# Kernel optimization log

Measured on AMD Instinct MI355X. Metric: run time of the kernel, lower is better.

Reference implementation:

```python
import jax, jax.numpy as jnp
import numpy as np

B, N, H, HEADS, PH, VD = 32, 256, 768, 12, 128, 16
DH = H // HEADS
VOCAB = 2 * VD + 3


def layer_norm(x, g, b, eps=1e-5):
    m = jnp.mean(x, axis=-1, keepdims=True)
    v = jnp.mean((x - m) ** 2, axis=-1, keepdims=True)
    return (x - m) * jax.lax.rsqrt(v + eps) * g + b


def setup_inputs() -> dict:
    key = jax.random.key(0)
    ks = jax.random.split(key, 12)
    # clamped relative-distance index pool, as in PathEmbeddingDistance
    t = np.arange(N)
    pool = t[None, :] - t[:, None]
    pool = np.clip(pool, -VD - 1, VD + 1) + VD + 1  # in [0, 2*VD+2]
    s = 0.02
    return {
        "nodes": jax.random.normal(ks[0], (B, N, H), jnp.float32),
        "bias": jnp.zeros((B, 1, 1, N), jnp.float32),
        "path_pool": jnp.asarray(pool, jnp.int32),
        "pos_table": jax.random.normal(ks[1], (VOCAB, PH), jnp.float32) * s,
        "Wq": jax.random.normal(ks[2], (H, H), jnp.float32) * s, "bq": jnp.zeros((H,), jnp.float32),
        "Wk": jax.random.normal(ks[3], (H, H), jnp.float32) * s, "bk": jnp.zeros((H,), jnp.float32),
        "Wv": jax.random.normal(ks[4], (H, H), jnp.float32) * s, "bv": jnp.zeros((H,), jnp.float32),
        "Wsk": jax.random.normal(ks[5], (PH, DH), jnp.float32) * s, "bsk": jnp.zeros((DH,), jnp.float32),
        "Wsv": jax.random.normal(ks[6], (PH, DH), jnp.float32) * s, "bsv": jnp.zeros((DH,), jnp.float32),
        "Wo": jax.random.normal(ks[7], (H, H), jnp.float32) * s, "bo": jnp.zeros((H,), jnp.float32),
        "g_path": jnp.ones((PH,), jnp.float32), "b_path": jnp.zeros((PH,), jnp.float32),
        "g_norm": jnp.ones((H,), jnp.float32), "b_norm": jnp.zeros((H,), jnp.float32),
    }


def reference(nodes, bias, path_pool, pos_table, Wq, bq, Wk, bk, Wv, bv,
              Wsk, bsk, Wsv, bsv, Wo, bo, g_path, b_path, g_norm, b_norm):
    # path embedding lookup (batch-independent: torch expand == broadcast)
    paths = pos_table[path_pool]                      # (N, N, PH)
    paths = layer_norm(paths, g_path, b_path)
    q = (nodes @ Wq + bq).reshape(B, N, HEADS, DH).transpose(0, 2, 1, 3)
    k = (nodes @ Wk + bk).reshape(B, N, HEADS, DH).transpose(0, 2, 1, 3)
    v = (nodes @ Wv + bv).reshape(B, N, HEADS, DH).transpose(0, 2, 1, 3)
    struct_k = paths @ Wsk + bsk                      # (N, N, DH)
    struct_v = paths @ Wsv + bsv                      # (N, N, DH)
    q = q * (DH ** -0.5)
    w = jnp.einsum("bhid,bhjd->bhij", q, k)
    struct_w = jnp.einsum("bhid,ijd->bhij", q, struct_k)
    w = jax.nn.softmax(w + struct_w + bias, axis=-1)  # (B, HEADS, N, N)
    out = jnp.einsum("bhij,bhjd->bhid", w, v) + jnp.einsum("bhij,ijd->bhid", w, struct_v)
    out = out.transpose(0, 2, 1, 3).reshape(B, N, H)  # combine heads
    out = jax.nn.relu(out @ Wo + bo)
    return layer_norm(nodes + out, g_norm, b_norm), w
```

## Files before the change

### kernel.cpp

```cpp
#include <hip/hip_runtime.h>
#include <hip/hip_bf16.h>

#define BB 32
#define NN 256
#define HH 768
#define NHEADS 12
#define DH 64
#define PHDIM 128
#define NVOCAB 35

typedef short bf16x8 __attribute__((ext_vector_type(8)));
typedef float f32x16 __attribute__((ext_vector_type(16)));
typedef unsigned u32x2 __attribute__((ext_vector_type(2)));

#define MFMA32 __builtin_amdgcn_mfma_f32_32x32x16_bf16

__device__ __forceinline__ unsigned short f2bf(float f) {
    unsigned u = __float_as_uint(f);
    unsigned r = (u + 0x7fffu + ((u >> 16) & 1u)) >> 16;
    return (unsigned short)r;
}

__device__ __forceinline__ unsigned pk2(float a, float b) {
    return (unsigned)f2bf(a) | ((unsigned)f2bf(b) << 16);
}

__device__ __forceinline__ bf16x8 pack8(const float f[8]) {
    bf16x8 r;
#pragma unroll
    for (int e = 0; e < 8; ++e) r[e] = (short)f2bf(f[e]);
    return r;
}

__global__ __launch_bounds__(256) void k_prep(
        const float* __restrict__ nodes, unsigned short* __restrict__ nodes_bf,
        const float* __restrict__ Wq, const float* __restrict__ Wk,
        const float* __restrict__ Wv, const float* __restrict__ Wo,
        unsigned short* __restrict__ Wt,
        const float* __restrict__ pos_table,
        const float* __restrict__ g_path, const float* __restrict__ b_path,
        const float* __restrict__ Wsk, const float* __restrict__ bsk,
        const float* __restrict__ Wsv, const float* __restrict__ bsv,
        unsigned short* __restrict__ skv_bf, unsigned short* __restrict__ svv_t_bf) {
    const int blk = blockIdx.x;
    const int tid = threadIdx.x;

    if (blk < 6144) {
        int i = (blk * 256 + tid) * 4;
        float4 v = *reinterpret_cast<const float4*>(&nodes[i]);
        ushort4 o;
        o.x = f2bf(v.x); o.y = f2bf(v.y); o.z = f2bf(v.z); o.w = f2bf(v.w);
        *reinterpret_cast<ushort4*>(&nodes_bf[i]) = o;
        return;
    }

    if (blk < 6720) {
        __shared__ unsigned short tile[64][72];
        int wb = blk - 6144;
        int z = wb / 144;
        int rem = wb - z * 144;
        int k0 = (rem / 12) * 64, c0 = (rem % 12) * 64;
        const float* W = (z == 0) ? Wq : (z == 1) ? Wk : (z == 2) ? Wv : Wo;
        unsigned short* out = Wt + (size_t)z * HH * HH;
#pragma unroll
        for (int l = 0; l < 16; ++l) {
            int e = tid + l * 256;
            int r = e >> 6, c = e & 63;
            tile[c][r] = f2bf(W[(size_t)(k0 + r) * HH + c0 + c]);
        }
        __syncthreads();
#pragma unroll
        for (int l = 0; l < 2; ++l) {
            int e = tid + l * 256;
            int c = e >> 3, ch = e & 7;
            *reinterpret_cast<bf16x8*>(&out[(size_t)(c0 + c) * HH + k0 + ch * 8]) =
                *reinterpret_cast<const bf16x8*>(&tile[c][ch * 8]);
        }
        return;
    }

    {
        int v = blk - 6720;
        int t = tid;
        if (v >= NVOCAB) {
            if (t < 64) skv_bf[v * 64 + t] = 0;
            else if (t < 128 && v < 48) svv_t_bf[(t - 64) * 48 + v] = 0;
            return;
        }
        __shared__ float x[PHDIM];
        __shared__ float red[PHDIM];
        float xv = 0.f;
        if (t < PHDIM) { xv = pos_table[v * PHDIM + t]; red[t] = xv; }
        __syncthreads();
        for (int s = 64; s > 0; s >>= 1) { if (t < s) red[t] += red[t + s]; __syncthreads(); }
        float mean = red[0] / PHDIM;
        __syncthreads();
        if (t < PHDIM) { float c = xv - mean; red[t] = c * c; }
        __syncthreads();
        for (int s = 64; s > 0; s >>= 1) { if (t < s) red[t] += red[t + s]; __syncthreads(); }
        float var = red[0] / PHDIM;
        __syncthreads();
        if (t < PHDIM) x[t] = (xv - mean) * rsqrtf(var + 1e-5f) * g_path[t] + b_path[t];
        __syncthreads();
        if (t < 64) {
            float acc = bsk[t];
            for (int p = 0; p < PHDIM; ++p) acc += x[p] * Wsk[p * DH + t];
            skv_bf[v * 64 + t] = f2bf(acc);
        } else if (t < 128) {
            int d = t - 64;
            float acc = bsv[d];
            for (int p = 0; p < PHDIM; ++p) acc += x[p] * Wsv[p * DH + d];
            svv_t_bf[d * 48 + v] = f2bf(acc);
        }
    }
}

__global__ __launch_bounds__(256) void k_qkv(
        const unsigned short* __restrict__ Abf, const unsigned short* __restrict__ Wt,
        const float* __restrict__ bq, const float* __restrict__ bk, const float* __restrict__ bv,
        unsigned short* __restrict__ q_bf, unsigned short* __restrict__ k_bf,
        unsigned short* __restrict__ v_bf_t) {
    __shared__ unsigned short Al[2][128 * 32];
    __shared__ unsigned short Bl[2][128 * 32];
    __shared__ unsigned short vstage[128][136];

    const int tid = threadIdx.x;
    const int w = tid >> 6, lane = tid & 63;
    const int il = lane & 31, hi = lane >> 5;
    const int wr = w >> 1, wc = w & 1;
    const int rowBase = blockIdx.x * 128;
    const int colBase = blockIdx.y * 128;
    const int sel = colBase / HH;
    const int jjBase0 = colBase - sel * HH;
    const float* bias = (sel == 0) ? bq : (sel == 1) ? bk : bv;

    f32x16 acc[2][2] = {};

    auto STAGE = [&](int buf, int k0) {
#pragma unroll
        for (int c = 0; c < 2; ++c) {
            int e = tid + c * 256;
            int row = e >> 2;
            int cb = (e & 3) << 4;
            int sc = cb ^ (((row >> 1) & 3) << 4);
            __builtin_amdgcn_global_load_lds(
                (const __attribute__((address_space(1))) unsigned int*)(Abf + (size_t)(rowBase + row) * HH + k0 + (sc >> 1)),
                (__attribute__((address_space(3))) unsigned int*)(&Al[buf][row * 32 + (cb >> 1)]), 16, 0, 0);
            __builtin_amdgcn_global_load_lds(
                (const __attribute__((address_space(1))) unsigned int*)(Wt + (size_t)(colBase + row) * HH + k0 + (sc >> 1)),
                (__attribute__((address_space(3))) unsigned int*)(&Bl[buf][row * 32 + (cb >> 1)]), 16, 0, 0);
        }
    };

    STAGE(0, 0);
    __syncthreads();
    for (int t = 0; t < 24; ++t) {
        int buf = t & 1;
        if (t < 23) STAGE(buf ^ 1, (t + 1) * 32);
#pragma unroll
        for (int ks = 0; ks < 2; ++ks) {
            bf16x8 af[2], bfr[2];
            int cb = (ks << 5) + (hi << 4);
#pragma unroll
            for (int t2 = 0; t2 < 2; ++t2) {
                int rrow = wr * 64 + t2 * 32 + il;
                af[t2] = *reinterpret_cast<const bf16x8*>(
                    &Al[buf][rrow * 32 + ((cb ^ (((rrow >> 1) & 3) << 4)) >> 1)]);
                int crow = wc * 64 + t2 * 32 + il;
                bfr[t2] = *reinterpret_cast<const bf16x8*>(
                    &Bl[buf][crow * 32 + ((cb ^ (((crow >> 1) & 3) << 4)) >> 1)]);
            }
            acc[0][0] = MFMA32(af[0], bfr[0], acc[0][0], 0, 0, 0);
            acc[0][1] = MFMA32(af[0], bfr[1], acc[0][1], 0, 0, 0);
            acc[1][0] = MFMA32(af[1], bfr[0], acc[1][0], 0, 0, 0);
            acc[1][1] = MFMA32(af[1], bfr[1], acc[1][1], 0, 0, 0);
        }
        __syncthreads();
    }

    if (sel < 2) {
        unsigned short* outp = (sel == 0) ? q_bf : k_bf;
        float scale = (sel == 0) ? 0.125f : 1.0f;
#pragma unroll
        for (int rt = 0; rt < 2; ++rt)
#pragma unroll
            for (int ct = 0; ct < 2; ++ct) {
                int jjB = jjBase0 + wc * 64 + ct * 32;
                int h = jjB >> 6;
                int d = ct * 32 + il;
                int kt = d >> 4, hif = (d >> 3) & 1, e = d & 7;
                float bias_v = bias[jjB + il];
#pragma unroll
                for (int r = 0; r < 16; ++r) {
                    int row = rowBase + wr * 64 + rt * 32 + ((r & 3) + 8 * (r >> 2) + 4 * hi);
                    int b = row >> 8, n = row & 255;
                    int jr = n & 31, t32 = n >> 5;
                    size_t off = ((((size_t)(b * NHEADS + h) * 8 + t32) * 4 + kt) * 64 +
                                  (hif * 32 + jr)) * 8 + e;
                    outp[off] = f2bf((acc[rt][ct][r] + bias_v) * scale);
                }
            }
    } else {
#pragma unroll
        for (int rt = 0; rt < 2; ++rt)
#pragma unroll
            for (int ct = 0; ct < 2; ++ct) {
                int jjB = jjBase0 + wc * 64 + ct * 32;
                float bias_v = bias[jjB + il];
#pragma unroll
                for (int r = 0; r < 16; ++r) {
                    int rl = wr * 64 + rt * 32 + ((r & 3) + 8 * (r >> 2) + 4 * hi);
                    vstage[wc * 64 + ct * 32 + il][rl] = f2bf(acc[rt][ct][r] + bias_v);
                }
            }
        __syncthreads();
        int b = rowBase >> 8, n0 = rowBase & 255;
        int h0 = jjBase0 >> 6;
#pragma unroll
        for (int l = 0; l < 8; ++l) {
            int idx = tid + l * 256;
            int cl = idx >> 4;
            int ch = idx & 15;
            int tl0 = ch * 8;
            int dg = cl & 63;
            int bh = b * NHEADS + h0 + (cl >> 6);
            int tok0 = n0 + tl0;
            int jt = tok0 >> 5, rem = tok0 & 31;
            int ks = rem >> 4, hif = (rem >> 3) & 1;
            int dh = dg >> 5;
            int lanef = hif * 32 + (dg & 31);
            size_t off = (((((size_t)bh * 8 + jt) * 2 + ks) * 2 + dh) * 64 + lanef) * 8;
            *reinterpret_cast<bf16x8*>(&v_bf_t[off]) =
                *reinterpret_cast<const bf16x8*>(&vstage[cl][tl0]);
        }
    }
}

__global__ __launch_bounds__(256, 4) void k_attn(
        const unsigned short* __restrict__ q_bf, const unsigned short* __restrict__ k_bf,
        const unsigned short* __restrict__ v_bf_t,
        const unsigned short* __restrict__ skv_bf, const unsigned short* __restrict__ svv_t_bf,
        const float* __restrict__ bias,
        float* __restrict__ wout, unsigned short* __restrict__ attn_out) {
    __shared__ __align__(16) float qs_s[32][36];
    __shared__ __align__(16) float wsum[32][48];
    __shared__ __align__(16) float oex[3][32][68];
    __shared__ float msum[4][32][2];
    __shared__ float bias_s[NN];

    const int bx0 = blockIdx.x;
    const int bx = (bx0 & 7) * 384 + (bx0 >> 3);
    const int bh = bx >> 3, rowblk = bx & 7;
    const int b = bh / NHEADS, h = bh - b * NHEADS;
    const int tid = threadIdx.x;
    const int w = tid >> 6, lane = tid & 63;
    const int il = lane & 31, hi = lane >> 5;
    const int i0 = rowblk * 32;
    const int ig = i0 + il;

    bias_s[tid] = bias[b * NN + tid];
#pragma unroll
    for (int z = 0; z < 6; ++z) ((float*)wsum)[tid + z * 256] = 0.f;

    bf16x8 qf[4];
#pragma unroll
    for (int kt = 0; kt < 4; ++kt)
        qf[kt] = *reinterpret_cast<const bf16x8*>(
            &q_bf[((((size_t)bh * 8 + rowblk) * 4 + kt) * 64 + lane) * 8]);

    if (w == 0) {
        f32x16 qa0 = {}, qa1 = {};
#pragma unroll
        for (int kt = 0; kt < 4; ++kt) {
            bf16x8 s0 = *reinterpret_cast<const bf16x8*>(&skv_bf[(size_t)il * 64 + kt * 16 + 8 * hi]);
            bf16x8 s1 = *reinterpret_cast<const bf16x8*>(&skv_bf[(size_t)(32 + il) * 64 + kt * 16 + 8 * hi]);
            qa0 = MFMA32(qf[kt], s0, qa0, 0, 0, 0);
            qa1 = MFMA32(qf[kt], s1, qa1, 0, 0, 0);
        }
#pragma unroll
        for (int r = 0; r < 16; ++r) {
            int ir = (r & 3) + 8 * (r >> 2) + 4 * hi;
            qs_s[ir][il] = qa0[r];
            if (il < 3) qs_s[ir][32 + il] = qa1[r];
        }
    }

    f32x16 S[2] = {};
#pragma unroll
    for (int jt = 0; jt < 2; ++jt) {
        int jtg = w * 2 + jt;
#pragma unroll
        for (int kt = 0; kt < 4; ++kt) {
            bf16x8 kf = *reinterpret_cast<const bf16x8*>(
                &k_bf[((((size_t)bh * 8 + jtg) * 4 + kt) * 64 + lane) * 8]);
            S[jt] = MFMA32(kf, qf[kt], S[jt], 0, 0, 0);
        }
    }

    __syncthreads();

    const int jb = w * 64;
    {
        float qlo = qs_s[il][0], qhi = qs_s[il][34];
#pragma unroll
        for (int jt = 0; jt < 2; ++jt) {
#pragma unroll
            for (int rg = 0; rg < 4; ++rg) {
                int j0 = jb + jt * 32 + rg * 8 + 4 * hi;
                float4 bv4 = *reinterpret_cast<const float4*>(&bias_s[j0]);
                float bvf[4] = {bv4.x, bv4.y, bv4.z, bv4.w};
#pragma unroll
                for (int e = 0; e < 4; ++e) {
                    int dd = j0 + e - ig;
                    float sw = (dd < -16) ? qlo : (dd > 16) ? qhi : qs_s[il][dd + 17];
                    S[jt][rg * 4 + e] += bvf[e] + sw;
                }
            }
        }
    }

    float m = -3.4e38f;
#pragma unroll
    for (int jt = 0; jt < 2; ++jt)
#pragma unroll
        for (int r = 0; r < 16; ++r) m = fmaxf(m, S[jt][r]);
    m = fmaxf(m, __shfl_xor(m, 32));
    float sum = 0.f;
#pragma unroll
    for (int jt = 0; jt < 2; ++jt)
#pragma unroll
        for (int r = 0; r < 16; ++r) { float p = __expf(S[jt][r] - m); S[jt][r] = p; sum += p; }
    sum += __shfl_xor(sum, 32);
    if (hi == 0) { msum[w][il][0] = m; msum[w][il][1] = sum; }
    __syncthreads();

    {
        float m0 = msum[0][il][0], m1 = msum[1][il][0];
        float m2 = msum[2][il][0], m3 = msum[3][il][0];
        float M = fmaxf(fmaxf(m0, m1), fmaxf(m2, m3));
        float sumT = msum[0][il][1] * __expf(m0 - M) + msum[1][il][1] * __expf(m1 - M) +
                     msum[2][il][1] * __expf(m2 - M) + msum[3][il][1] * __expf(m3 - M);
        float scale = __expf(m - M) / sumT;
#pragma unroll
        for (int jt = 0; jt < 2; ++jt)
#pragma unroll
            for (int r = 0; r < 16; ++r) S[jt][r] *= scale;
    }

#pragma unroll
    for (int jt = 0; jt < 2; ++jt) {
#pragma unroll
        for (int rg = 0; rg < 4; ++rg) {
            float4 val;
            val.x = S[jt][rg * 4 + 0];
            val.y = S[jt][rg * 4 + 1];
            val.z = S[jt][rg * 4 + 2];
            val.w = S[jt][rg * 4 + 3];
            *reinterpret_cast<float4*>(
                &wout[((size_t)(bh * NN + ig)) * NN + jb + jt * 32 + rg * 8 + 4 * hi]) = val;
        }
    }

    {
        float elo = 0.f, ehi = 0.f;
#pragma unroll
        for (int jt = 0; jt < 2; ++jt)
#pragma unroll
            for (int r = 0; r < 16; ++r) {
                int j = jb + jt * 32 + (r & 3) + 8 * (r >> 2) + 4 * hi;
                int dd = j - ig;
                float p = S[jt][r];
                if (dd < -16) elo += p;
                else if (dd > 16) ehi += p;
                else wsum[il][dd + 17] = p;
            }
        if (elo != 0.f) atomicAdd(&wsum[il][0], elo);
        if (ehi != 0.f) atomicAdd(&wsum[il][34], ehi);
    }

    f32x16 O0 = {}, O1 = {};
#pragma unroll
    for (int jt = 0; jt < 2; ++jt) {
        int jtg = w * 2 + jt;
#pragma unroll
        for (int ks = 0; ks < 2; ++ks) {
            unsigned w0 = pk2(S[jt][8 * ks + 0], S[jt][8 * ks + 1]);
            unsigned w1 = pk2(S[jt][8 * ks + 2], S[jt][8 * ks + 3]);
            unsigned w2 = pk2(S[jt][8 * ks + 4], S[jt][8 * ks + 5]);
            unsigned w3 = pk2(S[jt][8 * ks + 6], S[jt][8 * ks + 7]);
            unsigned s0 = hi ? w0 : w2, s1 = hi ? w1 : w3;
            unsigned y0 = (unsigned)__shfl_xor((int)s0, 32);
            unsigned y1 = (unsigned)__shfl_xor((int)s1, 32);
            union { bf16x8 v; unsigned u[4]; } Bf;
            Bf.u[0] = hi ? y0 : w0;
            Bf.u[1] = hi ? y1 : w1;
            Bf.u[2] = hi ? w2 : y0;
            Bf.u[3] = hi ? w3 : y1;
            bf16x8 va0 = *reinterpret_cast<const bf16x8*>(
                &v_bf_t[(((((size_t)bh * 8 + jtg) * 2 + ks) * 2 + 0) * 64 + lane) * 8]);
            bf16x8 va1 = *reinterpret_cast<const bf16x8*>(
                &v_bf_t[(((((size_t)bh * 8 + jtg) * 2 + ks) * 2 + 1) * 64 + lane) * 8]);
            O0 = MFMA32(va0, Bf.v, O0, 0, 0, 0);
            O1 = MFMA32(va1, Bf.v, O1, 0, 0, 0);
        }
    }

    if (w != 0) {
#pragma unroll
        for (int qq = 0; qq < 4; ++qq) {
            int d0 = 8 * qq + 4 * hi;
            *reinterpret_cast<float4*>(&oex[w - 1][il][d0]) =
                float4{O0[4 * qq + 0], O0[4 * qq + 1], O0[4 * qq + 2], O0[4 * qq + 3]};
            *reinterpret_cast<float4*>(&oex[w - 1][il][32 + d0]) =
                float4{O1[4 * qq + 0], O1[4 * qq + 1], O1[4 * qq + 2], O1[4 * qq + 3]};
        }
    }
    __syncthreads();

    if (w == 0) {
#pragma unroll
        for (int s = 0; s < 3; ++s) {
#pragma unroll
            for (int qq = 0; qq < 4; ++qq) {
                int d0 = 8 * qq + 4 * hi;
                float4 p0 = *reinterpret_cast<const float4*>(&oex[s][il][d0]);
                float4 p1 = *reinterpret_cast<const float4*>(&oex[s][il][32 + d0]);
                O0[4 * qq + 0] += p0.x; O0[4 * qq + 1] += p0.y;
                O0[4 * qq + 2] += p0.z; O0[4 * qq + 3] += p0.w;
                O1[4 * qq + 0] += p1.x; O1[4 * qq + 1] += p1.y;
                O1[4 * qq + 2] += p1.z; O1[4 * qq + 3] += p1.w;
            }
        }

#pragma unroll
        for (int kt = 0; kt < 3; ++kt) {
            float4 a0 = *reinterpret_cast<const float4*>(&wsum[il][kt * 16 + 8 * hi]);
            float4 a1 = *reinterpret_cast<const float4*>(&wsum[il][kt * 16 + 8 * hi + 4]);
            float af[8] = {a0.x, a0.y, a0.z, a0.w, a1.x, a1.y, a1.z, a1.w};
            bf16x8 Bf = pack8(af);
            bf16x8 sa0 = *reinterpret_cast<const bf16x8*>(&svv_t_bf[(size_t)il * 48 + kt * 16 + 8 * hi]);
            bf16x8 sa1 = *reinterpret_cast<const bf16x8*>(&svv_t_bf[(size_t)(32 + il) * 48 + kt * 16 + 8 * hi]);
            O0 = MFMA32(sa0, Bf, O0, 0, 0, 0);
            O1 = MFMA32(sa1, Bf, O1, 0, 0, 0);
        }

#pragma unroll
        for (int qq = 0; qq < 4; ++qq) {
            int d0 = 8 * qq + 4 * hi;
            u32x2 o0, o1;
            o0[0] = pk2(O0[4 * qq + 0], O0[4 * qq + 1]);
            o0[1] = pk2(O0[4 * qq + 2], O0[4 * qq + 3]);
            o1[0] = pk2(O1[4 * qq + 0], O1[4 * qq + 1]);
            o1[1] = pk2(O1[4 * qq + 2], O1[4 * qq + 3]);
            size_t base = ((size_t)(b * NN + i0 + il)) * HH + h * 64;
            *reinterpret_cast<u32x2*>(&attn_out[base + d0]) = o0;
            *reinterpret_cast<u32x2*>(&attn_out[base + 32 + d0]) = o1;
        }
    }
}

__global__ __launch_bounds__(256) void k_ogemm(
        const unsigned short* __restrict__ Abf, const unsigned short* __restrict__ Bt,
        const float* __restrict__ bo, unsigned short* __restrict__ Cout) {
    __shared__ unsigned short Al[2][128 * 32];
    __shared__ unsigned short Bl[2][128 * 32];

    const int tid = threadIdx.x;
    const int w = tid >> 6, lane = tid & 63;
    const int il = lane & 31, hi = lane >> 5;
    const int wr = w >> 1, wc = w & 1;
    const int rowBase = blockIdx.x * 128;
    const int colBase = blockIdx.y * 128;

    f32x16 acc[2][2] = {};

    auto STAGE = [&](int buf, int k0) {
#pragma unroll
        for (int c = 0; c < 2; ++c) {
            int e = tid + c * 256;
            int row = e >> 2;
            int cb = (e & 3) << 4;
            int sc = cb ^ (((row >> 1) & 3) << 4);
            __builtin_amdgcn_global_load_lds(
                (const __attribute__((address_space(1))) unsigned int*)(Abf + (size_t)(rowBase + row) * HH + k0 + (sc >> 1)),
                (__attribute__((address_space(3))) unsigned int*)(&Al[buf][row * 32 + (cb >> 1)]), 16, 0, 0);
            __builtin_amdgcn_global_load_lds(
                (const __attribute__((address_space(1))) unsigned int*)(Bt + (size_t)(colBase + row) * HH + k0 + (sc >> 1)),
                (__attribute__((address_space(3))) unsigned int*)(&Bl[buf][row * 32 + (cb >> 1)]), 16, 0, 0);
        }
    };

    STAGE(0, 0);
    __syncthreads();
    for (int t = 0; t < 24; ++t) {
        int buf = t & 1;
        if (t < 23) STAGE(buf ^ 1, (t + 1) * 32);
#pragma unroll
        for (int ks = 0; ks < 2; ++ks) {
            bf16x8 af[2], bfr[2];
            int cb = (ks << 5) + (hi << 4);
#pragma unroll
            for (int t2 = 0; t2 < 2; ++t2) {
                int rrow = wr * 64 + t2 * 32 + il;
                af[t2] = *reinterpret_cast<const bf16x8*>(
                    &Al[buf][rrow * 32 + ((cb ^ (((rrow >> 1) & 3) << 4)) >> 1)]);
                int crow = wc * 64 + t2 * 32 + il;
                bfr[t2] = *reinterpret_cast<const bf16x8*>(
                    &Bl[buf][crow * 32 + ((cb ^ (((crow >> 1) & 3) << 4)) >> 1)]);
            }
            acc[0][0] = MFMA32(af[0], bfr[0], acc[0][0], 0, 0, 0);
            acc[0][1] = MFMA32(af[0], bfr[1], acc[0][1], 0, 0, 0);
            acc[1][0] = MFMA32(af[1], bfr[0], acc[1][0], 0, 0, 0);
            acc[1][1] = MFMA32(af[1], bfr[1], acc[1][1], 0, 0, 0);
        }
        __syncthreads();
    }

#pragma unroll
    for (int rt = 0; rt < 2; ++rt)
#pragma unroll
        for (int ct = 0; ct < 2; ++ct) {
            int col = colBase + wc * 64 + ct * 32 + il;
            float bias_v = bo[col];
#pragma unroll
            for (int r = 0; r < 16; ++r) {
                int row = rowBase + wr * 64 + rt * 32 + ((r & 3) + 8 * (r >> 2) + 4 * hi);
                Cout[(size_t)row * HH + col] = f2bf(fmaxf(acc[rt][ct][r] + bias_v, 0.f));
            }
        }
}

__global__ __launch_bounds__(256) void k_ln(
        const float* __restrict__ nodes, const unsigned short* __restrict__ proj,
        const float* __restrict__ g, const float* __restrict__ bta,
        float* __restrict__ out) {
    __shared__ float red[2][4];
    int row = blockIdx.x;
    int tid = threadIdx.x;
    int w = tid >> 6, lane = tid & 63;
    float x[3];
    float s = 0.f, s2 = 0.f;
#pragma unroll
    for (int l = 0; l < 3; ++l) {
        int c = tid + l * 256;
        float pv = __uint_as_float(((unsigned)proj[(size_t)row * HH + c]) << 16);
        x[l] = nodes[(size_t)row * HH + c] + pv;
        s += x[l];
        s2 += x[l] * x[l];
    }
#pragma unroll
    for (int off = 32; off > 0; off >>= 1) {
        s += __shfl_xor(s, off);
        s2 += __shfl_xor(s2, off);
    }
    if (lane == 0) { red[0][w] = s; red[1][w] = s2; }
    __syncthreads();
    float ts = red[0][0] + red[0][1] + red[0][2] + red[0][3];
    float ts2 = red[1][0] + red[1][1] + red[1][2] + red[1][3];
    float mean = ts / HH;
    float var = ts2 / HH - mean * mean;
    float inv = rsqrtf(fmaxf(var, 0.f) + 1e-5f);
#pragma unroll
    for (int l = 0; l < 3; ++l) {
        int c = tid + l * 256;
        out[(size_t)row * HH + c] = (x[l] - mean) * inv * g[c] + bta[c];
    }
}

extern "C" void kernel_launch(void* const* d_in, const int* in_sizes, int n_in,
                              void* d_out, int out_size, void* d_ws, size_t ws_size,
                              hipStream_t stream) {
    const float* nodes     = (const float*)d_in[0];
    const float* bias      = (const float*)d_in[1];
    const float* pos_table = (const float*)d_in[3];
    const float* Wq = (const float*)d_in[4];  const float* bq = (const float*)d_in[5];
    const float* Wk = (const float*)d_in[6];  const float* bk = (const float*)d_in[7];
    const float* Wv = (const float*)d_in[8];  const float* bv = (const float*)d_in[9];
    const float* Wsk = (const float*)d_in[10]; const float* bsk = (const float*)d_in[11];
    const float* Wsv = (const float*)d_in[12]; const float* bsv = (const float*)d_in[13];
    const float* Wo = (const float*)d_in[14]; const float* bo = (const float*)d_in[15];
    const float* g_path = (const float*)d_in[16]; const float* b_path = (const float*)d_in[17];
    const float* g_norm = (const float*)d_in[18]; const float* b_norm = (const float*)d_in[19];

    float* out0 = (float*)d_out;
    float* wout = out0 + (size_t)BB * NN * HH;

    const size_t per = (size_t)BB * NN * HH;
    char* p = (char*)d_ws;
    unsigned short* q_bf    = (unsigned short*)p; p += per * 2;
    unsigned short* k_bf    = (unsigned short*)p; p += per * 2;
    unsigned short* v_bf_t  = (unsigned short*)p; p += per * 2;
    unsigned short* skv_bf  = (unsigned short*)p; p += 64 * 64 * 2;
    unsigned short* svv_t   = (unsigned short*)p; p += 64 * 48 * 2;
    unsigned short* nodes_bf= (unsigned short*)p; p += per * 2;
    unsigned short* Wt      = (unsigned short*)p; p += (size_t)4 * HH * HH * 2;
    unsigned short* attn_bf = (unsigned short*)p; p += per * 2;
    unsigned short* proj_bf = v_bf_t;

    k_prep<<<6784, 256, 0, stream>>>(nodes, nodes_bf, Wq, Wk, Wv, Wo, Wt,
                                     pos_table, g_path, b_path, Wsk, bsk, Wsv, bsv,
                                     skv_bf, svv_t);

    dim3 g2(64, 18);
    k_qkv<<<g2, 256, 0, stream>>>(nodes_bf, Wt, bq, bk, bv, q_bf, k_bf, v_bf_t);

    k_attn<<<BB * NHEADS * 8, 256, 0, stream>>>(q_bf, k_bf, v_bf_t, skv_bf, svv_t, bias, wout, attn_bf);

    dim3 g4(64, 6);
    k_ogemm<<<g4, 256, 0, stream>>>(attn_bf, Wt + (size_t)3 * HH * HH, bo, proj_bf);

    k_ln<<<BB * NN, 256, 0, stream>>>(nodes, proj_bf, g_norm, b_norm, out0);
}
```

Before: 149.1 us.

## Stage Q/K epilogue through LDS for vector stores, re-map V transpose writes, add setprio

The Q/K projection epilogue used to write scalar bf16 values straight into the MFMA-fragment layout in global memory. It now stages each 32x32 tile in shared memory (reusing vstage) and writes 16-byte vectors per lane, so global stores become coalesced. The V-transpose store loop is re-indexed so each wave writes a contiguous 512-element fragment block. The attention kernel also raises wave priority around its MFMA loops with s_setprio. The per-wave staging in vstage, which has no barrier between the LDS writes and reads, relies on each wave touching only its own region.

```diff
diff --git a/kernel.cpp b/kernel.cpp
--- a/kernel.cpp
+++ b/kernel.cpp
@@ -181,23 +181,30 @@
     if (sel < 2) {
         unsigned short* outp = (sel == 0) ? q_bf : k_bf;
         float scale = (sel == 0) ? 0.125f : 1.0f;
+        unsigned short* qst = &vstage[0][0];
+        const int b = rowBase >> 8;
+        const int hB = jjBase0 >> 6;
 #pragma unroll
         for (int rt = 0; rt < 2; ++rt)
 #pragma unroll
             for (int ct = 0; ct < 2; ++ct) {
                 int jjB = jjBase0 + wc * 64 + ct * 32;
-                int h = jjB >> 6;
-                int d = ct * 32 + il;
-                int kt = d >> 4, hif = (d >> 3) & 1, e = d & 7;
                 float bias_v = bias[jjB + il];
 #pragma unroll
                 for (int r = 0; r < 16; ++r) {
-                    int row = rowBase + wr * 64 + rt * 32 + ((r & 3) + 8 * (r >> 2) + 4 * hi);
-                    int b = row >> 8, n = row & 255;
-                    int jr = n & 31, t32 = n >> 5;
-                    size_t off = ((((size_t)(b * NHEADS + h) * 8 + t32) * 4 + kt) * 64 +
-                                  (hif * 32 + jr)) * 8 + e;
-                    outp[off] = f2bf((acc[rt][ct][r] + bias_v) * scale);
+                    int ir = (r & 3) + 8 * (r >> 2) + 4 * hi;
+                    qst[(w * 32 + ir) * 34 + il] = f2bf((acc[rt][ct][r] + bias_v) * scale);
+                }
+                int R0 = rowBase + wr * 64 + rt * 32;
+                int t32 = (R0 & 255) >> 5;
+                int bh = b * NHEADS + hB + wc;
+#pragma unroll
+                for (int g = 0; g < 2; ++g) {
+                    int kt = ct * 2 + g;
+                    size_t base = ((size_t)(bh * 8 + t32) * 4 + kt) * 512;
+                    bf16x8 vv = *reinterpret_cast<const bf16x8*>(
+                        &qst[(w * 32 + (lane & 31)) * 34 + g * 16 + (lane >> 5) * 8]);
+                    *reinterpret_cast<bf16x8*>(&outp[base + lane * 8]) = vv;
                 }
             }
     } else {
@@ -215,23 +222,17 @@
             }
         __syncthreads();
         int b = rowBase >> 8, n0 = rowBase & 255;
-        int h0 = jjBase0 >> 6;
-#pragma unroll
-        for (int l = 0; l < 8; ++l) {
-            int idx = tid + l * 256;
-            int cl = idx >> 4;
-            int ch = idx & 15;
-            int tl0 = ch * 8;
-            int dg = cl & 63;
-            int bh = b * NHEADS + h0 + (cl >> 6);
-            int tok0 = n0 + tl0;
-            int jt = tok0 >> 5, rem = tok0 & 31;
-            int ks = rem >> 4, hif = (rem >> 3) & 1;
-            int dh = dg >> 5;
-            int lanef = hif * 32 + (dg & 31);
-            size_t off = (((((size_t)bh * 8 + jt) * 2 + ks) * 2 + dh) * 64 + lanef) * 8;
-            *reinterpret_cast<bf16x8*>(&v_bf_t[off]) =
-                *reinterpret_cast<const bf16x8*>(&vstage[cl][tl0]);
+        int h0v = jjBase0 >> 6;
+#pragma unroll
+        for (int q = 0; q < 8; ++q) {
+            int rid = w * 8 + q;
+            int head = rid >> 4, jtl = (rid >> 2) & 3, ks = (rid >> 1) & 1, dh = rid & 1;
+            int bh = b * NHEADS + h0v + head;
+            int jtg = (n0 >> 5) + jtl;
+            size_t base = ((((size_t)(bh * 8 + jtg) * 2 + ks) * 2 + dh) * 64) * 8;
+            bf16x8 vv = *reinterpret_cast<const bf16x8*>(
+                &vstage[head * 64 + dh * 32 + (lane & 31)][jtl * 32 + ks * 16 + (lane >> 5) * 8]);
+            *reinterpret_cast<bf16x8*>(&v_bf_t[base + lane * 8]) = vv;
         }
     }
 }
@@ -286,6 +287,7 @@
     }
 
     f32x16 S[2] = {};
+    __builtin_amdgcn_s_setprio(1);
 #pragma unroll
     for (int jt = 0; jt < 2; ++jt) {
         int jtg = w * 2 + jt;
@@ -296,6 +298,7 @@
             S[jt] = MFMA32(kf, qf[kt], S[jt], 0, 0, 0);
         }
     }
+    __builtin_amdgcn_s_setprio(0);
 
     __syncthreads();
 
@@ -379,6 +382,7 @@
     }
 
     f32x16 O0 = {}, O1 = {};
+    __builtin_amdgcn_s_setprio(1);
 #pragma unroll
     for (int jt = 0; jt < 2; ++jt) {
         int jtg = w * 2 + jt;
@@ -404,6 +408,7 @@
             O1 = MFMA32(va1, Bf.v, O1, 0, 0, 0);
         }
     }
+    __builtin_amdgcn_s_setprio(0);
 
     if (w != 0) {
 #pragma unroll
```

Measured after the change: 143.9 us. 1.04x faster.
